# Kernel tuning notes

Measured on AMD Instinct MI355X. Metric: run time of the kernel, lower is better.

Reference implementation:

```python
import jax, jax.numpy as jnp
import numpy as np

N = 100000
E = 3200000
F_IN = 128
H = 64


def _glorot(key, fan_in, fan_out):
    lim = jnp.sqrt(6.0 / (fan_in + fan_out))
    return jax.random.uniform(key, (fan_in, fan_out), minval=-lim, maxval=lim, dtype=jnp.float32)


def setup_inputs() -> dict:
    key = jax.random.key(0)
    ks = jax.random.split(key, 16)
    x = jax.random.normal(ks[0], (N, F_IN), dtype=jnp.float32)
    edge_index = jax.random.randint(ks[1], (2, E), 0, N, dtype=jnp.int32)
    batch = jnp.zeros((N,), dtype=jnp.int32)
    dims = [(F_IN, H), (H, H // 2), (H // 2, H // 4), (H // 4, H // 2), (H // 2, H), (H, F_IN)]
    params = {}
    for i, (fi, fo) in enumerate(dims):
        params[f"W{i+1}"] = _glorot(ks[2 + i], fi, fo)
        params[f"b{i+1}"] = jnp.zeros((fo,), dtype=jnp.float32)
    params["Wf"] = _glorot(ks[10], F_IN, F_IN)
    params["bf"] = jnp.zeros((F_IN,), dtype=jnp.float32)
    return {"x": x, "edge_index": edge_index, "batch": batch, **params}


def _gcn_norm(edge_index, num_nodes):
    # PyG GCNConv: add self-loops, sym-normalize with deg^{-1/2}
    loop = jnp.arange(num_nodes, dtype=edge_index.dtype)
    row = jnp.concatenate([edge_index[0], loop])  # source j
    col = jnp.concatenate([edge_index[1], loop])  # target i
    deg = jax.ops.segment_sum(jnp.ones_like(col, dtype=jnp.float32), col, num_segments=num_nodes)
    dinv = jnp.where(deg > 0, jax.lax.rsqrt(deg), 0.0)
    norm = dinv[row] * dinv[col]
    return row, col, norm


def _gcn_conv(h, W, b, row, col, norm, num_nodes):
    h = h @ W  # linear first (no bias in lin), then normalized scatter-add
    msg = h[row] * norm[:, None]
    agg = jax.ops.segment_sum(msg, col, num_segments=num_nodes)
    return agg + b


def reference(x, edge_index, batch, W1, b1, W2, b2, W3, b3, W4, b4, W5, b5, W6, b6, Wf, bf):
    n = x.shape[0]
    row, col, norm = _gcn_norm(edge_index, n)
    h = jax.nn.relu(_gcn_conv(x, W1, b1, row, col, norm, n))
    h = jax.nn.relu(_gcn_conv(h, W2, b2, row, col, norm, n))
    h = jax.nn.relu(_gcn_conv(h, W3, b3, row, col, norm, n))
    h = jax.nn.relu(_gcn_conv(h, W4, b4, row, col, norm, n))
    h = jax.nn.relu(_gcn_conv(h, W5, b5, row, col, norm, n))
    h = jax.nn.relu(_gcn_conv(h, W6, b6, row, col, norm, n))
    return h @ Wf + bf
```

## Files before the change

### kernel.cpp

```cpp
#include <hip/hip_runtime.h>
#include <hip/hip_fp16.h>

#define BLK 256
#define NBSHIFT 7
#define MAXNB 800
#define GPART 512

typedef _Float16 half4v __attribute__((ext_vector_type(4)));
typedef _Float16 half8v __attribute__((ext_vector_type(8)));
typedef float    f32x4v __attribute__((ext_vector_type(4)));

__device__ __forceinline__ float4 ld4(const float* p) { return *(const float4*)p; }

__global__ __launch_bounds__(BLK) void p1_hist_k(const int* __restrict__ cols, int* __restrict__ hist,
                                                 int E, int nb) {
    __shared__ int h[MAXNB];
    const int tid = threadIdx.x, g = blockIdx.x;
    for (int b = tid; b < nb; b += BLK) h[b] = 0;
    __syncthreads();
    const int chunk = (E + GPART - 1) / GPART;
    const int start = g * chunk, end = min(E, start + chunk);
    for (int e = start + tid; e < end; e += BLK) atomicAdd(&h[cols[e] >> NBSHIFT], 1);
    __syncthreads();
    for (int b = tid; b < nb; b += BLK) hist[b * GPART + g] = h[b];
}
__global__ __launch_bounds__(256) void p2a_tot_k(const int* __restrict__ hist, int* __restrict__ tot) {
    __shared__ int s[256];
    const int b = blockIdx.x, t = threadIdx.x;
    s[t] = hist[b * GPART + t] + hist[b * GPART + 256 + t];
    __syncthreads();
    for (int o = 128; o > 0; o >>= 1) {
        if (t < o) s[t] += s[t + o];
        __syncthreads();
    }
    if (t == 0) tot[b] = s[0];
}
__global__ __launch_bounds__(256) void p2a_scan_k(const int* __restrict__ tot, int* __restrict__ bstart,
                                                  int nb, int E) {
    __shared__ int s[256];
    const int t = threadIdx.x;
    const int base = t * 4;
    int l0 = 0, l1 = 0, l2 = 0, l3 = 0;
    if (base < nb)     l0 = tot[base];
    if (base + 1 < nb) l1 = tot[base + 1];
    if (base + 2 < nb) l2 = tot[base + 2];
    if (base + 3 < nb) l3 = tot[base + 3];
    const int sum = l0 + l1 + l2 + l3;
    s[t] = sum;
    __syncthreads();
    for (int o = 1; o < 256; o <<= 1) {
        const int v = s[t] + ((t >= o) ? s[t - o] : 0);
        __syncthreads();
        s[t] = v;
        __syncthreads();
    }
    const int excl = s[t] - sum;
    if (base < nb)     bstart[base]     = excl;
    if (base + 1 < nb) bstart[base + 1] = excl + l0;
    if (base + 2 < nb) bstart[base + 2] = excl + l0 + l1;
    if (base + 3 < nb) bstart[base + 3] = excl + l0 + l1 + l2;
    if (t == 0) bstart[nb] = E;
}
__global__ __launch_bounds__(256) void p2b_k(int* __restrict__ hist, const int* __restrict__ bstart) {
    __shared__ int s[GPART];
    const int b = blockIdx.x, t = threadIdx.x;
    const int v0 = hist[b * GPART + t], v1 = hist[b * GPART + 256 + t];
    s[t] = v0; s[256 + t] = v1;
    __syncthreads();
    for (int o = 1; o < GPART; o <<= 1) {
        const int a0 = s[t] + ((t >= o) ? s[t - o] : 0);
        const int a1 = s[256 + t] + ((256 + t >= o) ? s[256 + t - o] : 0);
        __syncthreads();
        s[t] = a0; s[256 + t] = a1;
        __syncthreads();
    }
    const int base = bstart[b];
    hist[b * GPART + t] = base + s[t] - v0;
    hist[b * GPART + 256 + t] = base + s[256 + t] - v1;
}
__global__ __launch_bounds__(BLK) void p3_part_k(const int* __restrict__ rows, const int* __restrict__ cols,
                                                 const int* __restrict__ hist, int* __restrict__ pairs,
                                                 int E, int nb) {
    __shared__ int tail[MAXNB];
    const int tid = threadIdx.x, g = blockIdx.x;
    for (int b = tid; b < nb; b += BLK) tail[b] = hist[b * GPART + g];
    __syncthreads();
    const int chunk = (E + GPART - 1) / GPART;
    const int start = g * chunk, end = min(E, start + chunk);
    for (int e = start + tid; e < end; e += BLK) {
        const int r = rows[e], c = cols[e];
        const int pos = atomicAdd(&tail[c >> NBSHIFT], 1);
        pairs[pos] = ((c & ((1 << NBSHIFT) - 1)) << 17) | r;
    }
}
__global__ __launch_bounds__(BLK) void p4_fill_k(const int* __restrict__ pairs, const int* __restrict__ bstart,
                                                 int* __restrict__ P, float* __restrict__ dinv,
                                                 int* __restrict__ srow, int n) {
    constexpr int NN = 1 << NBSHIFT;
    __shared__ int dh[NN];
    __shared__ int tl[NN];
    const int b = blockIdx.x, t = threadIdx.x;
    const int base = b << NBSHIFT;
    const int nnod = min(NN, n - base);
    const int lo = bstart[b], hi = bstart[b + 1];
    if (t < NN) dh[t] = 0;
    __syncthreads();
    for (int e = lo + t; e < hi; e += BLK) atomicAdd(&dh[((unsigned)pairs[e]) >> 17], 1);
    __syncthreads();
    const int v0 = (t < NN) ? dh[t] : 0;
    if (t < NN) tl[t] = v0;
    __syncthreads();
    for (int o = 1; o < NN; o <<= 1) {
        int a0 = 0;
        if (t < NN) a0 = tl[t] + ((t >= o) ? tl[t - o] : 0);
        __syncthreads();
        if (t < NN) tl[t] = a0;
        __syncthreads();
    }
    const int s0 = lo + ((t < NN) ? tl[t] : 0) - v0;
    __syncthreads();
    if (t < NN) tl[t] = s0;
    if (t < nnod) { P[base + t] = s0; dinv[base + t] = rsqrtf((float)v0 + 1.0f); }
    __syncthreads();
    for (int e = lo + t; e < hi; e += BLK) {
        const int pv = pairs[e];
        const int pos = atomicAdd(&tl[((unsigned)pv) >> 17], 1);
        srow[pos] = pv & 0x1FFFF;
    }
}

__device__ __forceinline__ void addh(float2 A[4], const __half* p) {
    const float4 raw = ld4((const float*)p);
    const __half2* h = (const __half2*)&raw;
    const float2 f0 = __half22float2(h[0]);
    const float2 f1 = __half22float2(h[1]);
    const float2 f2 = __half22float2(h[2]);
    const float2 f3 = __half22float2(h[3]);
    A[0].x += f0.x; A[0].y += f0.y;
    A[1].x += f1.x; A[1].y += f1.y;
    A[2].x += f2.x; A[2].y += f2.y;
    A[3].x += f3.x; A[3].y += f3.y;
}

template<int WD, bool PRE, bool OUTH>
__global__ __launch_bounds__(BLK) void gatherh_k(const __half* __restrict__ Tp, const int* __restrict__ P,
                                                 const int* __restrict__ srow, const float* __restrict__ dinv,
                                                 const float* __restrict__ bin, void* __restrict__ outv,
                                                 int n, int E) {
    constexpr int LPN = WD / 8;
    const long gid = (long)blockIdx.x * BLK + threadIdx.x;
    const int i = (int)(gid / LPN);
    if (i >= n) return;
    const int q = (int)(gid % LPN) * 8;
    const int start = P[i];
    const int end = (i + 1 < n) ? P[i + 1] : E;
    const float d = dinv[i];
    const __half* __restrict__ Tq = Tp + q;
    float2 A0[4], A1[4], A2[4], A3[4];
    {
        const float4 raw = ld4((const float*)(Tq + (long)i * WD));
        const __half2* h = (const __half2*)&raw;
        A0[0] = __half22float2(h[0]); A0[1] = __half22float2(h[1]);
        A0[2] = __half22float2(h[2]); A0[3] = __half22float2(h[3]);
    }
#pragma unroll
    for (int k = 0; k < 4; k++) {
        A1[k] = make_float2(0.f, 0.f); A2[k] = make_float2(0.f, 0.f); A3[k] = make_float2(0.f, 0.f);
    }
    int e = start;
    const int ea = min(end, (start + 3) & ~3);
    for (; e < ea; e++) addh(A0, Tq + (long)srow[e] * WD);
    for (; e + 8 <= end; e += 8) {
        const int4 j0 = *(const int4*)&srow[e];
        const int4 j1 = *(const int4*)&srow[e + 4];
        addh(A0, Tq + (long)j0.x * WD); addh(A1, Tq + (long)j0.y * WD);
        addh(A2, Tq + (long)j0.z * WD); addh(A3, Tq + (long)j0.w * WD);
        addh(A0, Tq + (long)j1.x * WD); addh(A1, Tq + (long)j1.y * WD);
        addh(A2, Tq + (long)j1.z * WD); addh(A3, Tq + (long)j1.w * WD);
    }
    if (e + 4 <= end) {
        const int4 j0 = *(const int4*)&srow[e];
        addh(A0, Tq + (long)j0.x * WD); addh(A1, Tq + (long)j0.y * WD);
        addh(A2, Tq + (long)j0.z * WD); addh(A3, Tq + (long)j0.w * WD);
        e += 4;
    }
    for (; e < end; e++) addh(A0, Tq + (long)srow[e] * WD);
#pragma unroll
    for (int k = 0; k < 4; k++) {
        A0[k].x += A1[k].x + A2[k].x + A3[k].x;
        A0[k].y += A1[k].y + A2[k].y + A3[k].y;
    }
    float v[8];
    v[0] = d * A0[0].x; v[1] = d * A0[0].y; v[2] = d * A0[1].x; v[3] = d * A0[1].y;
    v[4] = d * A0[2].x; v[5] = d * A0[2].y; v[6] = d * A0[3].x; v[7] = d * A0[3].y;
    if (PRE) {
        const float4 b0 = ld4(&bin[q]);
        const float4 b1 = ld4(&bin[q + 4]);
        v[0] = fmaxf(v[0] + b0.x, 0.f) * d; v[1] = fmaxf(v[1] + b0.y, 0.f) * d;
        v[2] = fmaxf(v[2] + b0.z, 0.f) * d; v[3] = fmaxf(v[3] + b0.w, 0.f) * d;
        v[4] = fmaxf(v[4] + b1.x, 0.f) * d; v[5] = fmaxf(v[5] + b1.y, 0.f) * d;
        v[6] = fmaxf(v[6] + b1.z, 0.f) * d; v[7] = fmaxf(v[7] + b1.w, 0.f) * d;
    }
    if (OUTH) {
        const __half2 h0 = __floats2half2_rn(v[0], v[1]);
        const __half2 h1 = __floats2half2_rn(v[2], v[3]);
        const __half2 h2 = __floats2half2_rn(v[4], v[5]);
        const __half2 h3 = __floats2half2_rn(v[6], v[7]);
        uint4 u;
        u.x = *(const unsigned int*)&h0; u.y = *(const unsigned int*)&h1;
        u.z = *(const unsigned int*)&h2; u.w = *(const unsigned int*)&h3;
        *(uint4*)((__half*)outv + (long)i * WD + q) = u;
    } else {
        float* out = (float*)outv;
        float4 v0, v1;
        v0.x = v[0]; v0.y = v[1]; v0.z = v[2]; v0.w = v[3];
        v1.x = v[4]; v1.y = v[5]; v1.z = v[6]; v1.w = v[7];
        *(float4*)&out[(long)i * WD + q] = v0;
        *(float4*)&out[(long)i * WD + q + 4] = v1;
    }
}

template<int FI, int FO, bool INB, bool OUTB, bool OUTRELU, bool OSC, bool OUTH>
__global__ __launch_bounds__(BLK) void gemm_k(const float* __restrict__ H, const float* __restrict__ Wm,
                                              const float* __restrict__ bin, const float* __restrict__ bout,
                                              const float* __restrict__ dinv, float* __restrict__ out, int n) {
    constexpr int COLT = FO / 4;
    constexpr int RTH  = BLK / COLT;
    constexpr int RPT  = (FO >= 64) ? 8 : 4;
    constexpr int ROWS = RTH * RPT;
    constexpr int KC   = (FI > 64) ? 64 : FI;
    constexpr int NKB  = FI / KC;

    __shared__ float Wl[KC * FO];
    __shared__ float Hl[ROWS * (KC + 1)];

    const int tid    = threadIdx.x;
    const int colIdx = tid % COLT;
    const int rowIdx = tid / COLT;
    const long rowBase = (long)blockIdx.x * ROWS;

    float4 acc[RPT];
#pragma unroll
    for (int i = 0; i < RPT; i++) acc[i] = make_float4(0.f, 0.f, 0.f, 0.f);

    for (int kb = 0; kb < NKB; kb++) {
        if (kb) __syncthreads();
        for (int f = tid * 4; f < KC * FO; f += BLK * 4) {
            const int kr = f / FO, c = f % FO;
            *(float4*)&Wl[kr * FO + c] = ld4(&Wm[(kb * KC + kr) * FO + c]);
        }
        for (int f = tid * 4; f < ROWS * KC; f += BLK * 4) {
            const int rr = f / KC, kk = f % KC;
            const long r = rowBase + rr;
            float4 v = make_float4(0.f, 0.f, 0.f, 0.f);
            if (r < n) v = ld4(&H[r * FI + kb * KC + kk]);
            if (INB) {
                float4 b4 = ld4(&bin[kb * KC + kk]);
                v.x = fmaxf(v.x + b4.x, 0.f); v.y = fmaxf(v.y + b4.y, 0.f);
                v.z = fmaxf(v.z + b4.z, 0.f); v.w = fmaxf(v.w + b4.w, 0.f);
            }
            float* dst = &Hl[rr * (KC + 1) + kk];
            dst[0] = v.x; dst[1] = v.y; dst[2] = v.z; dst[3] = v.w;
        }
        __syncthreads();
#pragma unroll 8
        for (int k = 0; k < KC; k++) {
            const float4 w4 = *(const float4*)&Wl[k * FO + 4 * colIdx];
#pragma unroll
            for (int i = 0; i < RPT; i++) {
                const float hv = Hl[(rowIdx * RPT + i) * (KC + 1) + k];
                acc[i].x = fmaf(hv, w4.x, acc[i].x);
                acc[i].y = fmaf(hv, w4.y, acc[i].y);
                acc[i].z = fmaf(hv, w4.z, acc[i].z);
                acc[i].w = fmaf(hv, w4.w, acc[i].w);
            }
        }
    }

    float4 bo = make_float4(0.f, 0.f, 0.f, 0.f);
    if (OUTB) bo = ld4(&bout[4 * colIdx]);
#pragma unroll
    for (int i = 0; i < RPT; i++) {
        const long r = rowBase + rowIdx * RPT + i;
        if (r < n) {
            float4 v = acc[i];
            if (OUTB) { v.x += bo.x; v.y += bo.y; v.z += bo.z; v.w += bo.w; }
            if (OUTRELU) {
                v.x = fmaxf(v.x, 0.f); v.y = fmaxf(v.y, 0.f);
                v.z = fmaxf(v.z, 0.f); v.w = fmaxf(v.w, 0.f);
            }
            if (OSC) {
                const float d = dinv[r];
                v.x *= d; v.y *= d; v.z *= d; v.w *= d;
            }
            if (OUTH) {
                const __half2 h01 = __floats2half2_rn(v.x, v.y);
                const __half2 h23 = __floats2half2_rn(v.z, v.w);
                uint2 u;
                u.x = *(const unsigned int*)&h01;
                u.y = *(const unsigned int*)&h23;
                *(uint2*)((__half*)out + r * FO + 4 * colIdx) = u;
            } else {
                *(float4*)&out[r * FO + 4 * colIdx] = v;
            }
        }
    }
}

template<int K, int FO>
__global__ __launch_bounds__(BLK) void wprep_k(const float* __restrict__ Wm, _Float16* __restrict__ Wh) {
    const int f = (blockIdx.x * BLK + threadIdx.x) * 4;
    if (f >= K * FO) return;
    const int nn = f / K, k0 = f % K;
    const int blk = k0 & ~31, g = (k0 >> 2) & 3, h = (k0 >> 4) & 1;
    half4v w4;
#pragma unroll
    for (int c = 0; c < 4; c++) w4[c] = (_Float16)Wm[(k0 + c) * FO + nn];
    *(half4v*)&Wh[nn * K + blk + 8 * g + 4 * h] = w4;
}

template<int K, int FO, bool AH, bool OUTB, bool OUTRELU, bool OSC, bool OUTH>
__global__ __launch_bounds__(BLK) void mgemm_k(const void* __restrict__ Hv, const _Float16* __restrict__ Wh,
                                               const float* __restrict__ bout, const float* __restrict__ dinv,
                                               void* __restrict__ outv, int n) {
    constexpr int BM = 64;
    constexpr int KP = K + 8;
    constexpr int NT = FO / 16;
    __shared__ _Float16 Al[BM * KP];
    __shared__ _Float16 Bl[FO * KP];

    const int tid = threadIdx.x;
    const long rowBase = (long)blockIdx.x * BM;

    for (int f = tid * 8; f < K * FO; f += BLK * 8) {
        const int nn = f / K, k = f % K;
        *(uint4*)&Bl[nn * KP + k] = *(const uint4*)&Wh[f];
    }
    if (AH) {
        const __half* Hp = (const __half*)Hv;
        for (int f = tid * 8; f < BM * K; f += BLK * 8) {
            const int rr = f / K, k0 = f % K;
            const long r = rowBase + rr;
            uint4 u = make_uint4(0u, 0u, 0u, 0u);
            if (r < n) u = *(const uint4*)&Hp[r * K + k0];
            const int blk = k0 & ~31, g0 = (k0 >> 2) & 3, h = (k0 >> 4) & 1;
            *(uint2*)&Al[rr * KP + blk + 8 * g0 + 4 * h] = make_uint2(u.x, u.y);
            *(uint2*)&Al[rr * KP + blk + 8 * (g0 + 1) + 4 * h] = make_uint2(u.z, u.w);
        }
    } else {
        const float* Hp = (const float*)Hv;
        for (int f = tid * 4; f < BM * K; f += BLK * 4) {
            const int rr = f / K, k0 = f % K;
            const long r = rowBase + rr;
            float4 v = make_float4(0.f, 0.f, 0.f, 0.f);
            if (r < n) v = ld4(&Hp[r * K + k0]);
            const int blk = k0 & ~31, g = (k0 >> 2) & 3, h = (k0 >> 4) & 1;
            half4v a4;
            a4[0] = (_Float16)v.x; a4[1] = (_Float16)v.y; a4[2] = (_Float16)v.z; a4[3] = (_Float16)v.w;
            *(half4v*)&Al[rr * KP + blk + 8 * g + 4 * h] = a4;
        }
    }
    __syncthreads();

    const int wv = tid >> 6;
    const int lane = tid & 63;
    const int lr = lane & 15;
    const int lg = lane >> 4;
    const int wrow = wv * 16;

    const f32x4v vzero = {0.f, 0.f, 0.f, 0.f};
    f32x4v acc[NT];
#pragma unroll
    for (int t = 0; t < NT; t++) acc[t] = vzero;

#pragma unroll
    for (int ks = 0; ks < K / 32; ks++) {
        const int ko = ks * 32 + 8 * lg;
        const half8v a = *(const half8v*)&Al[(wrow + lr) * KP + ko];
#pragma unroll
        for (int nt = 0; nt < NT; nt++) {
            const half8v b = *(const half8v*)&Bl[(nt * 16 + lr) * KP + ko];
            acc[nt] = __builtin_amdgcn_mfma_f32_16x16x32_f16(a, b, acc[nt], 0, 0, 0);
        }
    }

    float bo[NT];
    if (OUTB) {
#pragma unroll
        for (int nt = 0; nt < NT; nt++) bo[nt] = bout[nt * 16 + lr];
    }
#pragma unroll
    for (int r = 0; r < 4; r++) {
        const long row = rowBase + wrow + lg * 4 + r;
        if (row < n) {
            const float d = OSC ? dinv[row] : 1.0f;
#pragma unroll
            for (int nt = 0; nt < NT; nt++) {
                float v = acc[nt][r];
                if (OUTB) v += bo[nt];
                if (OUTRELU) v = fmaxf(v, 0.f);
                if (OSC) v *= d;
                if (OUTH) ((__half*)outv)[row * FO + nt * 16 + lr] = __float2half_rn(v);
                else      ((float*)outv)[row * FO + nt * 16 + lr] = v;
            }
        }
    }
}

extern "C" void kernel_launch(void* const* d_in, const int* in_sizes, int n_in,
                              void* d_out, int out_size, void* d_ws, size_t ws_size,
                              hipStream_t stream)
{
    const float* x  = (const float*)d_in[0];
    const int*   ei = (const int*)d_in[1];
    const float* W1 = (const float*)d_in[3];  const float* b1 = (const float*)d_in[4];
    const float* W2 = (const float*)d_in[5];  const float* b2 = (const float*)d_in[6];
    const float* W3 = (const float*)d_in[7];  const float* b3 = (const float*)d_in[8];
    const float* W4 = (const float*)d_in[9];  const float* b4 = (const float*)d_in[10];
    const float* W5 = (const float*)d_in[11]; const float* b5 = (const float*)d_in[12];
    const float* W6 = (const float*)d_in[13]; const float* b6 = (const float*)d_in[14];
    const float* Wf = (const float*)d_in[15]; const float* bf = (const float*)d_in[16];

    const int n = in_sizes[0] / 128;
    const int E = in_sizes[1] / 2;
    const int* rows = ei;
    const int* cols = ei + E;

    int*   P    = (int*)d_ws;
    int*   srow = P + n;
    float* dinv = (float*)(srow + E);
    float* bufA = dinv + n;
    float* bufB = bufA + (size_t)n * 128;
    int*   pairs = (int*)bufA;
    int*   hist  = (int*)bufB;
    int*   bstart= hist + MAXNB * GPART;
    int*   tot   = bstart + 1032;
    _Float16* Wh1 = (_Float16*)(bufB + (size_t)n * 64);
    _Float16* Wh6 = Wh1 + 128 * 64;
    _Float16* Whf = Wh6 + 64 * 128;

    auto cdiv = [](long a, long b) { return (unsigned)((a + b - 1) / b); };
    const int nb = (n + (1 << NBSHIFT) - 1) >> NBSHIFT;

    wprep_k<128, 64><<<cdiv(128 * 64 / 4, BLK), BLK, 0, stream>>>(W1, Wh1);
    wprep_k<64, 128><<<cdiv(64 * 128 / 4, BLK), BLK, 0, stream>>>(W6, Wh6);
    wprep_k<128, 128><<<cdiv(128 * 128 / 4, BLK), BLK, 0, stream>>>(Wf, Whf);

    p1_hist_k<<<GPART, BLK, 0, stream>>>(cols, hist, E, nb);
    p2a_tot_k<<<nb, 256, 0, stream>>>(hist, tot);
    p2a_scan_k<<<1, 256, 0, stream>>>(tot, bstart, nb, E);
    p2b_k<<<nb, 256, 0, stream>>>(hist, bstart);
    p3_part_k<<<GPART, BLK, 0, stream>>>(rows, cols, hist, pairs, E, nb);
    p4_fill_k<<<nb, BLK, 0, stream>>>(pairs, bstart, P, dinv, srow, n);

    mgemm_k<128, 64, false, false, false, true, true><<<cdiv(n, 64), BLK, 0, stream>>>(x, Wh1, nullptr, dinv, bufA, n);
    gatherh_k<64, false, false><<<cdiv((long)n * 8, BLK), BLK, 0, stream>>>((const __half*)bufA, P, srow, dinv, nullptr, bufB, n, E);

    gemm_k<64, 32, true, false, false, true, true><<<cdiv(n, 128), BLK, 0, stream>>>(bufB, W2, b1, nullptr, dinv, bufA, n);
    gatherh_k<32, false, false><<<cdiv((long)n * 4, BLK), BLK, 0, stream>>>((const __half*)bufA, P, srow, dinv, nullptr, bufB, n, E);

    gemm_k<32, 16, true, false, false, true, true><<<cdiv(n, 256), BLK, 0, stream>>>(bufB, W3, b2, nullptr, dinv, bufA, n);
    gatherh_k<16, true, true><<<cdiv((long)n * 2, BLK), BLK, 0, stream>>>((const __half*)bufA, P, srow, dinv, b3, bufB, n, E);

    gatherh_k<16, false, false><<<cdiv((long)n * 2, BLK), BLK, 0, stream>>>((const __half*)bufB, P, srow, dinv, nullptr, bufA, n, E);
    gemm_k<16, 32, false, true, true, true, true><<<cdiv(n, 128), BLK, 0, stream>>>(bufA, W4, nullptr, b4, dinv, bufB, n);

    gatherh_k<32, false, false><<<cdiv((long)n * 4, BLK), BLK, 0, stream>>>((const __half*)bufB, P, srow, dinv, nullptr, bufA, n, E);
    gemm_k<32, 64, false, true, true, true, true><<<cdiv(n, 128), BLK, 0, stream>>>(bufA, W5, nullptr, b5, dinv, bufB, n);

    gatherh_k<64, false, true><<<cdiv((long)n * 8, BLK), BLK, 0, stream>>>((const __half*)bufB, P, srow, dinv, nullptr, bufA, n, E);
    mgemm_k<64, 128, true, true, true, false, true><<<cdiv(n, 64), BLK, 0, stream>>>(bufA, Wh6, b6, nullptr, bufB, n);

    mgemm_k<128, 128, true, true, false, false, false><<<cdiv(n, 64), BLK, 0, stream>>>(bufB, Whf, bf, nullptr, d_out, n);
}
```

Before: 598.2 us.

## Locally sort partition chunk in LDS before coalesced scatter to buckets

The partition kernel now recounts its chunk's bucket histogram, does a block-local prefix scan, and stages the packed pairs in shared memory sorted by bucket. It then writes them out in linear order with a per-bucket offset, so consecutive threads write contiguous runs instead of scattering single words to random global addresses. This adds a second pass over cols, a scan, and about 40KB of shared memory per block, and assumes each chunk has at most CMAX edges.

```diff
diff --git a/kernel.cpp b/kernel.cpp
--- a/kernel.cpp
+++ b/kernel.cpp
@@ -5,6 +5,7 @@
 #define NBSHIFT 7
 #define MAXNB 800
 #define GPART 512
+#define CMAX 6400
 
 typedef _Float16 half4v __attribute__((ext_vector_type(4)));
 typedef _Float16 half8v __attribute__((ext_vector_type(8)));
@@ -81,16 +82,59 @@
 __global__ __launch_bounds__(BLK) void p3_part_k(const int* __restrict__ rows, const int* __restrict__ cols,
                                                  const int* __restrict__ hist, int* __restrict__ pairs,
                                                  int E, int nb) {
-    __shared__ int tail[MAXNB];
+    __shared__ int h[MAXNB];
+    __shared__ int tailp[MAXNB];
+    __shared__ int delta[MAXNB];
+    __shared__ int sorted[CMAX];
+    __shared__ unsigned short bkt[CMAX];
+    __shared__ int s[256];
     const int tid = threadIdx.x, g = blockIdx.x;
-    for (int b = tid; b < nb; b += BLK) tail[b] = hist[b * GPART + g];
+    for (int b = tid; b < nb; b += BLK) h[b] = 0;
     __syncthreads();
     const int chunk = (E + GPART - 1) / GPART;
     const int start = g * chunk, end = min(E, start + chunk);
+    const int cnt = end - start;
+    for (int e = start + tid; e < end; e += BLK) atomicAdd(&h[cols[e] >> NBSHIFT], 1);
+    __syncthreads();
+    {
+        const int base = tid * 4;
+        int l0 = 0, l1 = 0, l2 = 0, l3 = 0;
+        if (base < nb)     l0 = h[base];
+        if (base + 1 < nb) l1 = h[base + 1];
+        if (base + 2 < nb) l2 = h[base + 2];
+        if (base + 3 < nb) l3 = h[base + 3];
+        const int sum = l0 + l1 + l2 + l3;
+        s[tid] = sum;
+        __syncthreads();
+        for (int o = 1; o < 256; o <<= 1) {
+            const int v = s[tid] + ((tid >= o) ? s[tid - o] : 0);
+            __syncthreads();
+            s[tid] = v;
+            __syncthreads();
+        }
+        const int excl = s[tid] - sum;
+        if (base < nb)     h[base]     = excl;
+        if (base + 1 < nb) h[base + 1] = excl + l0;
+        if (base + 2 < nb) h[base + 2] = excl + l0 + l1;
+        if (base + 3 < nb) h[base + 3] = excl + l0 + l1 + l2;
+    }
+    __syncthreads();
+    for (int b = tid; b < nb; b += BLK) {
+        const int ls = h[b];
+        tailp[b] = ls;
+        delta[b] = hist[b * GPART + g] - ls;
+    }
+    __syncthreads();
     for (int e = start + tid; e < end; e += BLK) {
         const int r = rows[e], c = cols[e];
-        const int pos = atomicAdd(&tail[c >> NBSHIFT], 1);
-        pairs[pos] = ((c & ((1 << NBSHIFT) - 1)) << 17) | r;
+        const int b = c >> NBSHIFT;
+        const int lpos = atomicAdd(&tailp[b], 1);
+        sorted[lpos] = ((c & ((1 << NBSHIFT) - 1)) << 17) | r;
+        bkt[lpos] = (unsigned short)b;
+    }
+    __syncthreads();
+    for (int i = tid; i < cnt; i += BLK) {
+        pairs[delta[bkt[i]] + i] = sorted[i];
     }
 }
 __global__ __launch_bounds__(BLK) void p4_fill_k(const int* __restrict__ pairs, const int* __restrict__ bstart,
```

Measured after the change: 566.9 us. 1.06x faster.
